# Optimization experiments

Measured on AMD Instinct MI355X. Metric: run time of the kernel, lower is better.

Reference implementation:

```python
import jax, jax.numpy as jnp
import numpy as np
import math

CHANNELS = 1024
NUM_HEADS = 16
HEAD_DIM = CHANNELS // NUM_HEADS  # 64
ROPE_DIM = int(HEAD_DIM * 0.5)    # 32
BASE_FREQ = 10000.0


def apply_rope(x):
    """x: [b, h, t, d]; rotate first ROPE_DIM features, pass the rest through."""
    t = x.shape[2]
    half = ROPE_DIM // 2
    theta = 1.0 / (BASE_FREQ ** (jnp.arange(0, ROPE_DIM, 2, dtype=jnp.float32) / ROPE_DIM))  # [half]
    ang = jnp.arange(t, dtype=jnp.float32)[:, None] * theta[None, :]  # [t, half]
    ang = jnp.concatenate([ang, ang], axis=-1)  # [t, ROPE_DIM]
    cos = jnp.cos(ang)[None, None, :, :]
    sin = jnp.sin(ang)[None, None, :, :]
    x_rope, x_pass = x[..., :ROPE_DIM], x[..., ROPE_DIM:]
    neg_half = jnp.concatenate([-x_rope[..., half:], x_rope[..., :half]], axis=-1)
    x_rope = x_rope * cos + neg_half * sin
    return jnp.concatenate([x_rope, x_pass], axis=-1)


def proximal_bias(length):
    pos = jnp.arange(length, dtype=jnp.float32)
    diff = pos[None, :] - pos[:, None]
    return -jnp.log1p(jnp.abs(diff))[None, None, :, :]  # [1,1,t,t]


def conv1x1(x, w, b):
    """x: [b, c_in, t], w: [c_out, c_in], b: [c_out] -> [b, c_out, t]"""
    return jnp.einsum('oc,bct->bot', w, x) + b[None, :, None]


def setup_inputs() -> dict:
    key = jax.random.key(0)
    ks = jax.random.split(key, 10)
    B, C, T = 8, CHANNELS, 1024
    scale = 1.0 / math.sqrt(C)
    return {
        "x": jax.random.normal(ks[0], (B, C, T), dtype=jnp.float32),
        "context": jax.random.normal(ks[1], (B, C, T), dtype=jnp.float32),
        "attention_mask": jnp.ones((B, 1, 1, T), dtype=jnp.int32),
        "Wq": jax.random.normal(ks[2], (C, C), dtype=jnp.float32) * scale,
        "bq": jnp.zeros((C,), dtype=jnp.float32),
        "Wk": jax.random.normal(ks[3], (C, C), dtype=jnp.float32) * scale,
        "bk": jnp.zeros((C,), dtype=jnp.float32),
        "Wv": jax.random.normal(ks[4], (C, C), dtype=jnp.float32) * scale,
        "bv": jnp.zeros((C,), dtype=jnp.float32),
        "Wo": jax.random.normal(ks[5], (C, C), dtype=jnp.float32) * scale,
        "bo": jnp.zeros((C,), dtype=jnp.float32),
    }


def reference(x, context, attention_mask, Wq, bq, Wk, bk, Wv, bv, Wo, bo):
    B, C, T = x.shape
    H, D = NUM_HEADS, HEAD_DIM
    q = conv1x1(x, Wq, bq)
    k = conv1x1(context, Wk, bk)
    v = conv1x1(context, Wv, bv)
    # b (h d) t -> b h t d
    def split_heads(z):
        return z.reshape(B, H, D, -1).transpose(0, 1, 3, 2)
    q, k, v = split_heads(q), split_heads(k), split_heads(v)
    q = apply_rope(q)
    k = apply_rope(k)
    scores = jnp.einsum('bhqd,bhkd->bhqk', q, k) / math.sqrt(D)
    scores = scores + proximal_bias(T)  # proximal_bias=True, self-attention
    scores = jnp.where(attention_mask == 0, jnp.float32(-10000.0), scores)
    probs = jax.nn.softmax(scores, axis=-1)  # dropout_rate=0.0 -> identity
    out = jnp.einsum('bhqk,bhkd->bhqd', probs, v)
    # b h q d -> b (h d) q
    out = out.transpose(0, 1, 3, 2).reshape(B, C, T)
    return conv1x1(out, Wo, bo)
```

## Files before the change

kernel.cpp:

```cpp
#include <hip/hip_runtime.h>
#include <hip/hip_bf16.h>
#include <math.h>

#define BB 8
#define CC 1024
#define TT 1024
#define HH 16
#define DD 64

typedef __attribute__((ext_vector_type(8))) short short8;
typedef __attribute__((ext_vector_type(4))) short short4_;
typedef __attribute__((ext_vector_type(4))) float f32x4;
typedef __attribute__((ext_vector_type(4))) int   i32x4;
typedef __attribute__((ext_vector_type(2))) unsigned long long u64x2;

#define QSCALE 0.18033688f

__device__ __forceinline__ unsigned short f2bf(float f) {
    unsigned u = __builtin_bit_cast(unsigned, f);
    u += 0x7fffu + ((u >> 16) & 1u);
    return (unsigned short)(u >> 16);
}

__device__ __forceinline__ f32x4 mfma16(short8 a, short8 b, f32x4 c) {
    return __builtin_amdgcn_mfma_f32_16x16x32_bf16(a, b, c, 0, 0, 0);
}

__device__ __forceinline__ void async16(const void* g, void* l) {
    __builtin_amdgcn_global_load_lds(
        (const __attribute__((address_space(1))) unsigned int*)g,
        (__attribute__((address_space(3))) unsigned int*)l, 16, 0, 0);
}

__device__ __forceinline__ unsigned cvtpk(float lo, float hi) {
    unsigned r;
    asm("v_cvt_pk_bf16_f32 %0, %1, %2" : "=v"(r) : "v"(lo), "v"(hi));
    return r;
}

__global__ __launch_bounds__(256) void cast_w_kernel(
    const float* __restrict__ Wq, const float* __restrict__ Wk,
    const float* __restrict__ Wv, const float* __restrict__ Wo,
    unsigned short* __restrict__ dst)
{
    const int z = blockIdx.y;
    const float* W = (z == 0) ? Wq : (z == 1) ? Wk : (z == 2) ? Wv : Wo;
    unsigned short* d = dst + (size_t)z * CC * CC;
    int idx = blockIdx.x * 256 + threadIdx.x;
    float4 f = ((const float4*)W)[idx];
    short4_ s;
    s[0] = (short)f2bf(f.x); s[1] = (short)f2bf(f.y);
    s[2] = (short)f2bf(f.z); s[3] = (short)f2bf(f.w);
    ((short4_*)d)[idx] = s;
}

__global__ __launch_bounds__(256) void tcast2_kernel(
    const float* __restrict__ x, const float* __restrict__ ctx,
    unsigned short* __restrict__ xT, unsigned short* __restrict__ cTo)
{
    __shared__ float sT[64][65];
    const int tid = threadIdx.x;
    const int z = blockIdx.z;
    const float* in = (z < BB) ? x : ctx;
    unsigned short* out = (z < BB) ? xT : cTo;
    const int b = (z < BB) ? z : z - BB;
    const int tB = blockIdx.x * 64, cT = blockIdx.y * 64;

    const float* ib = in + ((size_t)b * CC + cT) * TT + tB;
    const int r = tid >> 2;
    #pragma unroll
    for (int j = 0; j < 4; j++) {
        int t4 = (tid & 3) * 4 + j * 16;
        float4 f = *(const float4*)(ib + (size_t)r * TT + t4);
        sT[r][t4 + 0] = f.x; sT[r][t4 + 1] = f.y;
        sT[r][t4 + 2] = f.z; sT[r][t4 + 3] = f.w;
    }
    __syncthreads();
    const int t_l = tid >> 2, cch = (tid & 3) * 16;
    short8 o0, o1;
    #pragma unroll
    for (int i = 0; i < 8; i++) {
        o0[i] = (short)f2bf(sT[cch + i][t_l]);
        o1[i] = (short)f2bf(sT[cch + 8 + i][t_l]);
    }
    unsigned short* dp = out + ((size_t)b * TT + tB + t_l) * CC + cT + cch;
    *(short8*)dp = o0;
    *(short8*)(dp + 8) = o1;
}

__global__ __launch_bounds__(256) void tcast_kernel(
    const float* __restrict__ in, unsigned short* __restrict__ out)
{
    __shared__ float sT[64][65];
    const int tid = threadIdx.x;
    const int tB = blockIdx.x * 64, cT = blockIdx.y * 64, b = blockIdx.z;

    const float* ib = in + ((size_t)b * CC + cT) * TT + tB;
    const int r = tid >> 2;
    #pragma unroll
    for (int j = 0; j < 4; j++) {
        int t4 = (tid & 3) * 4 + j * 16;
        float4 f = *(const float4*)(ib + (size_t)r * TT + t4);
        sT[r][t4 + 0] = f.x; sT[r][t4 + 1] = f.y;
        sT[r][t4 + 2] = f.z; sT[r][t4 + 3] = f.w;
    }
    __syncthreads();
    const int t_l = tid >> 2, cch = (tid & 3) * 16;
    short8 o0, o1;
    #pragma unroll
    for (int i = 0; i < 8; i++) {
        o0[i] = (short)f2bf(sT[cch + i][t_l]);
        o1[i] = (short)f2bf(sT[cch + 8 + i][t_l]);
    }
    unsigned short* dp = out + ((size_t)b * TT + tB + t_l) * CC + cT + cch;
    *(short8*)dp = o0;
    *(short8*)(dp + 8) = o1;
}

__global__ __launch_bounds__(256) void qkv_gll_kernel(
    const unsigned short* __restrict__ xT, const unsigned short* __restrict__ cT,
    const unsigned short* __restrict__ Wq2, const unsigned short* __restrict__ Wk2,
    const unsigned short* __restrict__ Wv2,
    const float* __restrict__ bq, const float* __restrict__ bk,
    const float* __restrict__ bv,
    unsigned short* __restrict__ qo, unsigned short* __restrict__ ko,
    unsigned short* __restrict__ vo,
    int mode)
{
    __shared__ __align__(16) short smem[4 * 64 * 72];
    short* sA = smem;
    short* sB = smem + 4096;

    const int tid = threadIdx.x, lane = tid & 63, wave = tid >> 6;
    const int wm = wave >> 1, wn = wave & 1;
    const int l15 = lane & 15, lq = lane >> 4;

    const int tTile = blockIdx.x, oTile = blockIdx.y;
    const int zz = blockIdx.z;
    int w, b;
    if (mode == 0)      { w = zz % 3;        b = zz / 3;  }
    else if (mode == 1) { w = 0;             b = zz;      }
    else                { w = 1 + (zz & 1);  b = zz >> 1; }
    const unsigned short* inT = (w == 0) ? xT : cT;
    const int oBase = oTile * 128, tBase = tTile * 128;

    const unsigned short* WA = (w == 0) ? Wq2 : (w == 1) ? Wk2 : Wv2;
    const float* bias        = (w == 0) ? bq  : (w == 1) ? bk  : bv;

    const int srow = lane >> 2;
    const int sch  = (lane ^ (lane >> 2) ^ (lane >> 4)) & 3;
    const unsigned short* gA0 = WA + (size_t)(oBase + wave * 32 + srow) * CC + sch * 8;
    const unsigned short* gA1 = gA0 + (size_t)16 * CC;
    const unsigned short* gB0 = inT + ((size_t)b * TT + tBase + wave * 32 + srow) * CC + sch * 8;
    const unsigned short* gB1 = gB0 + (size_t)16 * CC;
    short* lA0 = sA + (wave * 2 + 0) * 512;
    short* lA1 = sA + (wave * 2 + 1) * 512;
    short* lB0 = sB + (wave * 2 + 0) * 512;
    short* lB1 = sB + (wave * 2 + 1) * 512;

    const int csw = ((lq ^ (l15 & 3) ^ (l15 >> 2)) & 3) * 8;

    f32x4 acc[4][4];
    #pragma unroll
    for (int mt = 0; mt < 4; mt++)
        #pragma unroll
        for (int nt = 0; nt < 4; nt++) acc[mt][nt] = (f32x4){0.f, 0.f, 0.f, 0.f};

    for (int c0 = 0; c0 < CC; c0 += 32) {
        async16(gA0 + c0, lA0);
        async16(gA1 + c0, lA1);
        async16(gB0 + c0, lB0);
        async16(gB1 + c0, lB1);
        __syncthreads();

        short8 af[4], bf[4];
        #pragma unroll
        for (int mt = 0; mt < 4; mt++)
            af[mt] = *(short8*)(sA + (wm * 64 + mt * 16 + l15) * 32 + csw);
        #pragma unroll
        for (int nt = 0; nt < 4; nt++)
            bf[nt] = *(short8*)(sB + (wn * 64 + nt * 16 + l15) * 32 + csw);
        #pragma unroll
        for (int mt = 0; mt < 4; mt++)
            #pragma unroll
            for (int nt = 0; nt < 4; nt++)
                acc[mt][nt] = mfma16(af[mt], bf[nt], acc[mt][nt]);
        __syncthreads();
    }

    #pragma unroll
    for (int mt = 0; mt < 4; mt++)
        #pragma unroll
        for (int r = 0; r < 4; r++) {
            float bi = bias[oBase + wm * 64 + mt * 16 + lq * 4 + r];
            #pragma unroll
            for (int nt = 0; nt < 4; nt++) {
                acc[mt][nt][r] += bi;
                if (w == 0) acc[mt][nt][r] *= QSCALE;
            }
        }

    const int h = oTile * 2 + wm;
    short* sT = smem + wave * (64 * 72);

    if (w < 2) {
        #pragma unroll
        for (int r = 0; r < 4; r++) {
            float dr = (float)(lq * 4 + r);
            float theta = exp2f(dr * -0.8304820237f);
            float sa, ca, ss, cs;
            sincosf((float)(tBase + wn * 64 + l15) * theta, &sa, &ca);
            sincosf(16.0f * theta, &ss, &cs);
            #pragma unroll
            for (int nt = 0; nt < 4; nt++) {
                float x0 = acc[0][nt][r], x1 = acc[1][nt][r];
                acc[0][nt][r] = x0 * ca - x1 * sa;
                acc[1][nt][r] = x1 * ca + x0 * sa;
                float c2 = ca * cs - sa * ss;
                sa = sa * cs + ca * ss;
                ca = c2;
            }
        }
        #pragma unroll
        for (int nt = 0; nt < 4; nt++)
            #pragma unroll
            for (int mt = 0; mt < 4; mt++) {
                short4_ v4;
                #pragma unroll
                for (int r = 0; r < 4; r++) v4[r] = (short)f2bf(acc[mt][nt][r]);
                *(short4_*)(sT + (nt * 16 + l15) * 72 + mt * 16 + lq * 4) = v4;
            }
    } else {
        #pragma unroll
        for (int mt = 0; mt < 4; mt++)
            #pragma unroll
            for (int r = 0; r < 4; r++)
                #pragma unroll
                for (int nt = 0; nt < 4; nt++)
                    sT[(mt * 16 + lq * 4 + r) * 72 + nt * 16 + l15] =
                        (short)f2bf(acc[mt][nt][r]);
    }
    __asm__ volatile("s_waitcnt lgkmcnt(0)" ::: "memory");

    unsigned short* dstBase;
    if (w == 0)
        dstBase = qo + ((size_t)(b * HH + h) * TT + tBase + wn * 64 + lane) * DD;
    else if (w == 1)
        dstBase = ko + ((size_t)(b * HH + h) * TT + tBase + wn * 64 + lane) * DD;
    else
        dstBase = vo + ((size_t)(b * HH + h) * DD + lane) * TT + tBase + wn * 64;
    #pragma unroll
    for (int j = 0; j < 8; j++)
        *(short8*)(dstBase + j * 8) = *(short8*)(sT + lane * 72 + j * 8);
}

__global__ __launch_bounds__(256) void oproj_gll_kernel(
    const unsigned short* __restrict__ att, const unsigned short* __restrict__ Wo2,
    const float* __restrict__ bo, float* __restrict__ out)
{
    __shared__ __align__(16) short smem[8192];
    short* sA = smem;
    short* sB = smem + 4096;

    const int tid = threadIdx.x, lane = tid & 63, wave = tid >> 6;
    const int wm = wave >> 1, wn = wave & 1;
    const int l15 = lane & 15, lq = lane >> 4;
    const int tTile = blockIdx.x, oTile = blockIdx.y, b = blockIdx.z;
    const int oBase = oTile * 128, tBase = tTile * 128;

    const int srow = lane >> 2;
    const int sch  = (lane ^ (lane >> 2) ^ (lane >> 4)) & 3;
    const unsigned short* gA0 = Wo2 + (size_t)(oBase + wave * 32 + srow) * CC + sch * 8;
    const unsigned short* gA1 = gA0 + (size_t)16 * CC;
    const unsigned short* attB = att + (size_t)b * HH * TT * DD;
    const int t0 = tBase + wave * 32 + srow;
    short* lA0 = sA + (wave * 2 + 0) * 512;
    short* lA1 = sA + (wave * 2 + 1) * 512;
    short* lB0 = sB + (wave * 2 + 0) * 512;
    short* lB1 = sB + (wave * 2 + 1) * 512;

    const int csw = ((lq ^ (l15 & 3) ^ (l15 >> 2)) & 3) * 8;

    f32x4 acc[4][4];
    #pragma unroll
    for (int mt = 0; mt < 4; mt++)
        #pragma unroll
        for (int nt = 0; nt < 4; nt++) acc[mt][nt] = (f32x4){0.f, 0.f, 0.f, 0.f};

    for (int c0 = 0; c0 < CC; c0 += 32) {
        int c = c0 + sch * 8;
        const unsigned short* g0 =
            attB + ((size_t)(c >> 6) * TT + t0) * DD + (c & 63);
        async16(gA0 + c0, lA0);
        async16(gA1 + c0, lA1);
        async16(g0, lB0);
        async16(g0 + 16 * DD, lB1);
        __syncthreads();

        short8 af[4], bf[4];
        #pragma unroll
        for (int mt = 0; mt < 4; mt++)
            af[mt] = *(short8*)(sA + (wm * 64 + mt * 16 + l15) * 32 + csw);
        #pragma unroll
        for (int nt = 0; nt < 4; nt++)
            bf[nt] = *(short8*)(sB + (wn * 64 + nt * 16 + l15) * 32 + csw);
        #pragma unroll
        for (int mt = 0; mt < 4; mt++)
            #pragma unroll
            for (int nt = 0; nt < 4; nt++)
                acc[mt][nt] = mfma16(af[mt], bf[nt], acc[mt][nt]);
        __syncthreads();
    }

    #pragma unroll
    for (int mt = 0; mt < 4; mt++)
        #pragma unroll
        for (int r = 0; r < 4; r++) {
            int o = oBase + wm * 64 + mt * 16 + lq * 4 + r;
            float bi = bo[o];
            float* dst = out + ((size_t)b * CC + o) * TT + tBase + wn * 64;
            #pragma unroll
            for (int nt = 0; nt < 4; nt++)
                dst[nt * 16 + l15] = acc[mt][nt][r] + bi;
        }
}

__global__ __launch_bounds__(256) void attn_mfma_kernel(
    const unsigned short* __restrict__ q, const unsigned short* __restrict__ k,
    const unsigned short* __restrict__ v, const int* __restrict__ mask,
    unsigned short* __restrict__ att)
{
    __shared__ __align__(16) short sQw[64 * 72];
    __shared__ __align__(16) short sK[64 * 72];
    __shared__ __align__(16) short sV[64 * 72];
    __shared__ int sOK[4];

    const int tid = threadIdx.x, lane = tid & 63, wq = tid >> 6;
    const int l15 = lane & 15, lq = lane >> 4;
    const int qTile = blockIdx.x, bh = blockIdx.y, b = bh >> 4;

    const int sr = tid >> 2, sc = (tid & 3) * 16;
    const int* maskB = mask + b * TT;

    {
        i32x4 m4 = *(const i32x4*)(maskB + tid * 4);
        int ok = (m4[0] != 0) & (m4[1] != 0) & (m4[2] != 0) & (m4[3] != 0);
        unsigned long long bal = __ballot(ok);
        if (lane == 0) sOK[wq] = (bal == ~0ull);
    }

    {
        const unsigned short* gq = q + ((size_t)bh * TT + qTile * 64 + sr) * DD + sc;
        *(short8*)(sQw + sr * 72 + sc)     = *(const short8*)gq;
        *(short8*)(sQw + sr * 72 + sc + 8) = *(const short8*)(gq + 8);
    }
    __syncthreads();

    const short8 bq0 = *(short8*)(sQw + (wq * 16 + l15) * 72 + lq * 8);
    const short8 bq1 = *(short8*)(sQw + (wq * 16 + l15) * 72 + 32 + lq * 8);
    const bool allOK = sOK[0] && sOK[1] && sOK[2] && sOK[3];
    __syncthreads();

    float* wtab = (float*)sQw;
    #pragma unroll
    for (int j = 0; j < 8; j++) {
        int d = tid + 256 * j;
        int ad = d - 1023; ad = ad < 0 ? -ad : ad;
        wtab[d] = __builtin_amdgcn_rcpf(1.0f + (float)ad);
    }

    short8 vones;
    #pragma unroll
    for (int e = 0; e < 8; e++) vones[e] = (short)0x3F80;

    f32x4 accO[4];
    #pragma unroll
    for (int nt = 0; nt < 4; nt++) accO[nt] = (f32x4){0.f, 0.f, 0.f, 0.f};
    f32x4 accD = (f32x4){0.f, 0.f, 0.f, 0.f};

    const int qpos = qTile * 64 + wq * 16 + l15;
    const unsigned short* kB = k + (size_t)bh * TT * DD;
    const unsigned short* vB = v + (size_t)bh * DD * TT;

    const int xo = ((tid & 3) >> 1) * 8 + (tid & 1) * 4;
    short* vwp = sV + sr * 72 + xo;

    const unsigned short* gk = kB + (size_t)sr * DD + sc;
    const unsigned short* gv = vB + (size_t)sr * TT + sc;
    short8 kr0 = *(const short8*)gk;
    short8 kr1 = *(const short8*)(gk + 8);
    short8 vr0 = *(const short8*)gv;
    short8 vr1 = *(const short8*)(gv + 8);

    for (int kt = 0; kt < 16; kt++) {
        __syncthreads();
        *(short8*)(sK + sr * 72 + sc)     = kr0;
        *(short8*)(sK + sr * 72 + sc + 8) = kr1;
        {
            u64x2 vv0 = __builtin_bit_cast(u64x2, vr0);
            u64x2 vv1 = __builtin_bit_cast(u64x2, vr1);
            *(unsigned long long*)(vwp)      = vv0[0];
            *(unsigned long long*)(vwp + 16) = vv0[1];
            *(unsigned long long*)(vwp + 32) = vv1[0];
            *(unsigned long long*)(vwp + 48) = vv1[1];
        }
        __syncthreads();

        if (kt < 15) {
            gk += 64 * DD;
            gv += 64;
            kr0 = *(const short8*)gk;
            kr1 = *(const short8*)(gk + 8);
            vr0 = *(const short8*)gv;
            vr1 = *(const short8*)(gv + 8);
        }

        f32x4 s4[4];
        #pragma unroll
        for (int nt = 0; nt < 4; nt++) {
            short8 ka0 = *(short8*)(sK + (nt * 16 + l15) * 72 + lq * 8);
            short8 ka1 = *(short8*)(sK + (nt * 16 + l15) * 72 + 32 + lq * 8);
            f32x4 z = (f32x4){0.f, 0.f, 0.f, 0.f};
            z = mfma16(ka0, bq0, z);
            z = mfma16(ka1, bq1, z);
            s4[nt] = z;
        }

        const float* wrow = wtab + (kt * 64 + lq * 4 + 1023 - qpos);
        unsigned pk8[4][2];
        if (allOK) {
            #pragma unroll
            for (int nt = 0; nt < 4; nt++) {
                #pragma unroll
                for (int h2 = 0; h2 < 2; h2++) {
                    float p0 = __builtin_amdgcn_exp2f(s4[nt][2 * h2])
                               * wrow[nt * 16 + 2 * h2];
                    float p1 = __builtin_amdgcn_exp2f(s4[nt][2 * h2 + 1])
                               * wrow[nt * 16 + 2 * h2 + 1];
                    pk8[nt][h2] = cvtpk(p0, p1);
                }
            }
        } else {
            #pragma unroll
            for (int nt = 0; nt < 4; nt++) {
                i32x4 mk = *(const i32x4*)(maskB + kt * 64 + nt * 16 + lq * 4);
                #pragma unroll
                for (int h2 = 0; h2 < 2; h2++) {
                    float p0 = __builtin_amdgcn_exp2f(s4[nt][2 * h2])
                               * wrow[nt * 16 + 2 * h2];
                    float p1 = __builtin_amdgcn_exp2f(s4[nt][2 * h2 + 1])
                               * wrow[nt * 16 + 2 * h2 + 1];
                    p0 = mk[2 * h2]     ? p0 : 0.f;
                    p1 = mk[2 * h2 + 1] ? p1 : 0.f;
                    pk8[nt][h2] = cvtpk(p0, p1);
                }
            }
        }

        i32x4 c0 = {(int)pk8[0][0], (int)pk8[0][1], (int)pk8[1][0], (int)pk8[1][1]};
        i32x4 c1 = {(int)pk8[2][0], (int)pk8[2][1], (int)pk8[3][0], (int)pk8[3][1]};
        short8 ap0 = __builtin_bit_cast(short8, c0);
        short8 ap1 = __builtin_bit_cast(short8, c1);

        accD = mfma16(ap0, vones, accD);
        accD = mfma16(ap1, vones, accD);

        #pragma unroll
        for (int nt = 0; nt < 4; nt++) {
            const short* vrow = sV + (nt * 16 + l15) * 72 + lq * 16;
            short8 b0 = *(short8*)(vrow);
            short8 b1 = *(short8*)(vrow + 8);
            accO[nt] = mfma16(ap0, b0, accO[nt]);
            accO[nt] = mfma16(ap1, b1, accO[nt]);
        }
    }

    unsigned short* aB = att + ((size_t)bh * TT + qTile * 64 + wq * 16 + lq * 4) * DD;
    #pragma unroll
    for (int r = 0; r < 4; r++) {
        float inv = 1.0f / accD[r];
        #pragma unroll
        for (int nt = 0; nt < 4; nt++)
            aB[(size_t)r * DD + nt * 16 + l15] = f2bf(accO[nt][r] * inv);
    }
}

__global__ __launch_bounds__(256) void qkv_mfma_kernel(
    const float* __restrict__ x, const float* __restrict__ ctx,
    const float* __restrict__ Wq, const float* __restrict__ bq,
    const float* __restrict__ Wk, const float* __restrict__ bk,
    const float* __restrict__ Wv, const float* __restrict__ bv,
    unsigned short* __restrict__ qo, unsigned short* __restrict__ ko,
    unsigned short* __restrict__ vo)
{
    __shared__ __align__(16) short smem[4 * 64 * 72];
    short* sA = smem;
    short* sB = smem + 128 * 40;

    const int tid  = threadIdx.x;
    const int lane = tid & 63;
    const int wave = tid >> 6;
    const int wm = wave >> 1, wn = wave & 1;
    const int l15 = lane & 15, lq = lane >> 4;

    const int tTile = blockIdx.x, oTile = blockIdx.y;
    const int b = blockIdx.z / 3, w = blockIdx.z % 3;
    const int oBase = oTile * 128, tBase = tTile * 128;

    const float* In   = (w == 0) ? x  : ctx;
    const float* W    = (w == 0) ? Wq : (w == 1) ? Wk : Wv;
    const float* bias = (w == 0) ? bq : (w == 1) ? bk : bv;
    const float* InB  = In + (size_t)b * CC * TT;

    const int ao = tid >> 1, ak = (tid & 1) * 16;
    const int bt = tid & 127, bk_ = (tid >> 7) * 16;
    const float* gA = W + (size_t)(oBase + ao) * CC + ak;
    const float* gB = InB + (size_t)bk_ * TT + tBase + bt;

    f32x4 acc[4][4];
    #pragma unroll
    for (int mt = 0; mt < 4; mt++)
        #pragma unroll
        for (int nt = 0; nt < 4; nt++) acc[mt][nt] = (f32x4){0.f, 0.f, 0.f, 0.f};

    for (int c0 = 0; c0 < CC; c0 += 32) {
        float fa[16], fb[16];
        #pragma unroll
        for (int i = 0; i < 4; i++) {
            float4 t4 = *(const float4*)(gA + c0 + 4 * i);
            fa[4*i+0] = t4.x; fa[4*i+1] = t4.y; fa[4*i+2] = t4.z; fa[4*i+3] = t4.w;
        }
        #pragma unroll
        for (int j = 0; j < 16; j++)
            fb[j] = gB[(size_t)(c0 + j) * TT];

        __syncthreads();
        short8 pa0, pa1, pb0, pb1;
        #pragma unroll
        for (int e = 0; e < 8; e++) {
            pa0[e] = (short)f2bf(fa[e]);   pa1[e] = (short)f2bf(fa[8 + e]);
            pb0[e] = (short)f2bf(fb[e]);   pb1[e] = (short)f2bf(fb[8 + e]);
        }
        *(short8*)(sA + ao * 40 + ak)     = pa0;
        *(short8*)(sA + ao * 40 + ak + 8) = pa1;
        *(short8*)(sB + bt * 40 + bk_)     = pb0;
        *(short8*)(sB + bt * 40 + bk_ + 8) = pb1;
        __syncthreads();

        short8 af[4], bf[4];
        #pragma unroll
        for (int mt = 0; mt < 4; mt++)
            af[mt] = *(short8*)(sA + (wm * 64 + mt * 16 + l15) * 40 + lq * 8);
        #pragma unroll
        for (int nt = 0; nt < 4; nt++)
            bf[nt] = *(short8*)(sB + (wn * 64 + nt * 16 + l15) * 40 + lq * 8);
        #pragma unroll
        for (int mt = 0; mt < 4; mt++)
            #pragma unroll
            for (int nt = 0; nt < 4; nt++)
                acc[mt][nt] = mfma16(af[mt], bf[nt], acc[mt][nt]);
    }

    #pragma unroll
    for (int mt = 0; mt < 4; mt++)
        #pragma unroll
        for (int r = 0; r < 4; r++) {
            float bi = bias[oBase + wm * 64 + mt * 16 + lq * 4 + r];
            #pragma unroll
            for (int nt = 0; nt < 4; nt++) {
                acc[mt][nt][r] += bi;
                if (w == 0) acc[mt][nt][r] *= QSCALE;
            }
        }

    const int h = oTile * 2 + wm;
    __syncthreads();
    short* sT = smem + wave * (64 * 72);

    if (w < 2) {
        #pragma unroll
        for (int r = 0; r < 4; r++) {
            float theta = powf(10000.0f, -(float)(lq * 4 + r) * (1.0f / 16.0f));
            #pragma unroll
            for (int nt = 0; nt < 4; nt++) {
                float tpos = (float)(tBase + wn * 64 + nt * 16 + l15);
                float sa, ca;
                sincosf(tpos * theta, &sa, &ca);
                float x0 = acc[0][nt][r], x1 = acc[1][nt][r];
                acc[0][nt][r] = x0 * ca - x1 * sa;
                acc[1][nt][r] = x1 * ca + x0 * sa;
            }
        }
        #pragma unroll
        for (int nt = 0; nt < 4; nt++)
            #pragma unroll
            for (int mt = 0; mt < 4; mt++) {
                short4_ v4;
                #pragma unroll
                for (int r = 0; r < 4; r++) v4[r] = (short)f2bf(acc[mt][nt][r]);
                *(short4_*)(sT + (nt * 16 + l15) * 72 + mt * 16 + lq * 4) = v4;
            }
    } else {
        #pragma unroll
        for (int mt = 0; mt < 4; mt++)
            #pragma unroll
            for (int r = 0; r < 4; r++)
                #pragma unroll
                for (int nt = 0; nt < 4; nt++)
                    sT[(mt * 16 + lq * 4 + r) * 72 + nt * 16 + l15] =
                        (short)f2bf(acc[mt][nt][r]);
    }
    __asm__ volatile("s_waitcnt lgkmcnt(0)" ::: "memory");

    unsigned short* dstBase;
    if (w == 0)
        dstBase = qo + ((size_t)(b * HH + h) * TT + tBase + wn * 64 + lane) * DD;
    else if (w == 1)
        dstBase = ko + ((size_t)(b * HH + h) * TT + tBase + wn * 64 + lane) * DD;
    else
        dstBase = vo + ((size_t)(b * HH + h) * DD + lane) * TT + tBase + wn * 64;
    #pragma unroll
    for (int j = 0; j < 8; j++)
        *(short8*)(dstBase + j * 8) = *(short8*)(sT + lane * 72 + j * 8);
}

__global__ __launch_bounds__(256) void oproj_mfma_kernel(
    const unsigned short* __restrict__ att, const float* __restrict__ Wo,
    const float* __restrict__ bo, float* __restrict__ out)
{
    __shared__ __align__(16) short smem[2 * 128 * 40];
    short* sA = smem;
    short* sB = smem + 128 * 40;

    const int tid = threadIdx.x, lane = tid & 63, wave = tid >> 6;
    const int wm = wave >> 1, wn = wave & 1;
    const int l15 = lane & 15, lq = lane >> 4;
    const int tTile = blockIdx.x, oTile = blockIdx.y, b = blockIdx.z;
    const int oBase = oTile * 128, tBase = tTile * 128;

    const int ao = tid >> 1, ak = (tid & 1) * 16;
    const int bt = tid & 127, bk_ = (tid >> 7) * 16;
    const float* gA = Wo + (size_t)(oBase + ao) * CC + ak;

    f32x4 acc[4][4];
    #pragma unroll
    for (int mt = 0; mt < 4; mt++)
        #pragma unroll
        for (int nt = 0; nt < 4; nt++) acc[mt][nt] = (f32x4){0.f, 0.f, 0.f, 0.f};

    for (int c0 = 0; c0 < CC; c0 += 32) {
        float fa[16];
        #pragma unroll
        for (int i = 0; i < 4; i++) {
            float4 t4 = *(const float4*)(gA + c0 + 4 * i);
            fa[4*i+0] = t4.x; fa[4*i+1] = t4.y; fa[4*i+2] = t4.z; fa[4*i+3] = t4.w;
        }
        int c = c0 + bk_;
        const unsigned short* gB =
            att + (((size_t)b * HH + (c >> 6)) * TT + tBase + bt) * DD + (c & 63);
        short8 pb0 = *(const short8*)gB;
        short8 pb1 = *(const short8*)(gB + 8);

        __syncthreads();
        short8 pa0, pa1;
        #pragma unroll
        for (int e = 0; e < 8; e++) {
            pa0[e] = (short)f2bf(fa[e]); pa1[e] = (short)f2bf(fa[8 + e]);
        }
        *(short8*)(sA + ao * 40 + ak)      = pa0;
        *(short8*)(sA + ao * 40 + ak + 8)  = pa1;
        *(short8*)(sB + bt * 40 + bk_)     = pb0;
        *(short8*)(sB + bt * 40 + bk_ + 8) = pb1;
        __syncthreads();

        short8 af[4], bf[4];
        #pragma unroll
        for (int mt = 0; mt < 4; mt++)
            af[mt] = *(short8*)(sA + (wm * 64 + mt * 16 + l15) * 40 + lq * 8);
        #pragma unroll
        for (int nt = 0; nt < 4; nt++)
            bf[nt] = *(short8*)(sB + (wn * 64 + nt * 16 + l15) * 40 + lq * 8);
        #pragma unroll
        for (int mt = 0; mt < 4; mt++)
            #pragma unroll
            for (int nt = 0; nt < 4; nt++)
                acc[mt][nt] = mfma16(af[mt], bf[nt], acc[mt][nt]);
    }

    #pragma unroll
    for (int mt = 0; mt < 4; mt++)
        #pragma unroll
        for (int r = 0; r < 4; r++) {
            int o = oBase + wm * 64 + mt * 16 + lq * 4 + r;
            float bi = bo[o];
            float* dst = out + ((size_t)b * CC + o) * TT + tBase + wn * 64;
            #pragma unroll
            for (int nt = 0; nt < 4; nt++)
                dst[nt * 16 + l15] = acc[mt][nt][r] + bi;
        }
}

extern "C" void kernel_launch(void* const* d_in, const int* in_sizes, int n_in,
                              void* d_out, int out_size, void* d_ws, size_t ws_size,
                              hipStream_t stream)
{
    const float* x   = (const float*)d_in[0];
    const float* ctx = (const float*)d_in[1];
    const int* mask  = (const int*)d_in[2];
    const float* Wq  = (const float*)d_in[3];
    const float* bq  = (const float*)d_in[4];
    const float* Wk  = (const float*)d_in[5];
    const float* bk  = (const float*)d_in[6];
    const float* Wv  = (const float*)d_in[7];
    const float* bv  = (const float*)d_in[8];
    const float* Wo  = (const float*)d_in[9];
    const float* bo  = (const float*)d_in[10];
    float* out = (float*)d_out;

    const size_t nq = (size_t)BB * HH * TT * DD;
    const size_t nw = (size_t)CC * CC;

    if (ws_size >= (5 * nq + 4 * nw) * sizeof(unsigned short)) {
        unsigned short* q   = (unsigned short*)d_ws;
        unsigned short* k   = q + nq;
        unsigned short* v   = k + nq;
        unsigned short* xT  = v + nq;
        unsigned short* cT  = xT + nq;
        unsigned short* Wb  = cT + nq;
        unsigned short* Wqb = Wb;
        unsigned short* Wkb = Wb + nw;
        unsigned short* Wvb = Wb + 2 * nw;
        unsigned short* Wob = Wb + 3 * nw;

        cast_w_kernel<<<dim3(1024, 4), 256, 0, stream>>>(Wq, Wk, Wv, Wo, Wb);
        tcast2_kernel<<<dim3(16, 16, BB * 2), 256, 0, stream>>>(x, ctx, xT, cT);
        qkv_gll_kernel<<<dim3(8, 8, BB * 3), 256, 0, stream>>>(
            xT, cT, Wqb, Wkb, Wvb, bq, bk, bv, q, k, v, 0);
        attn_mfma_kernel<<<dim3(TT / 64, BB * HH), 256, 0, stream>>>(
            q, k, v, mask, xT);
        oproj_gll_kernel<<<dim3(8, 8, BB), 256, 0, stream>>>(xT, Wob, bo, out);
    } else if (ws_size >= (4 * nq + 4 * nw) * sizeof(unsigned short)) {
        unsigned short* q   = (unsigned short*)d_ws;
        unsigned short* k   = q + nq;
        unsigned short* v   = k + nq;
        unsigned short* buf = v + nq;
        unsigned short* Wb  = buf + nq;
        unsigned short* Wqb = Wb;
        unsigned short* Wkb = Wb + nw;
        unsigned short* Wvb = Wb + 2 * nw;
        unsigned short* Wob = Wb + 3 * nw;

        cast_w_kernel<<<dim3(1024, 4), 256, 0, stream>>>(Wq, Wk, Wv, Wo, Wb);
        tcast_kernel<<<dim3(16, 16, BB), 256, 0, stream>>>(x, buf);
        qkv_gll_kernel<<<dim3(8, 8, BB), 256, 0, stream>>>(
            buf, buf, Wqb, Wkb, Wvb, bq, bk, bv, q, k, v, 1);
        tcast_kernel<<<dim3(16, 16, BB), 256, 0, stream>>>(ctx, buf);
        qkv_gll_kernel<<<dim3(8, 8, BB * 2), 256, 0, stream>>>(
            buf, buf, Wqb, Wkb, Wvb, bq, bk, bv, q, k, v, 2);
        attn_mfma_kernel<<<dim3(TT / 64, BB * HH), 256, 0, stream>>>(
            q, k, v, mask, buf);
        oproj_gll_kernel<<<dim3(8, 8, BB), 256, 0, stream>>>(buf, Wob, bo, out);
    } else {
        unsigned short* q   = (unsigned short*)d_ws;
        unsigned short* k   = q + nq;
        unsigned short* v   = k + nq;
        unsigned short* att = v + nq;
        qkv_mfma_kernel<<<dim3(8, 8, BB * 3), 256, 0, stream>>>(
            x, ctx, Wq, bq, Wk, bk, Wv, bv, q, k, v);
        attn_mfma_kernel<<<dim3(TT / 64, BB * HH), 256, 0, stream>>>(
            q, k, v, mask, att);
        oproj_mfma_kernel<<<dim3(8, 8, BB), 256, 0, stream>>>(att, Wo, bo, out);
    }
}
```

Baseline: 304.1 us.

## Double-buffer LDS tiles in QKV and output projection GEMMs

Both projection GEMM kernels now use two LDS buffers per operand: the next K-slice is prefetched with async global-to-LDS loads while the current slice is consumed by MFMA, and buffers are swapped after a single barrier per iteration. This is meant to overlap global memory latency with compute instead of stalling on a barrier right after each load. It doubles LDS use in the output projection kernel, which may reduce occupancy, and correctness depends on the async loads completing before the next barrier.

After: 307.9 us. No clear change (+1.2%).

```diff
diff --git a/kernel.cpp b/kernel.cpp
--- a/kernel.cpp
+++ b/kernel.cpp
@@ -128,8 +128,6 @@
     int mode)
 {
     __shared__ __align__(16) short smem[4 * 64 * 72];
-    short* sA = smem;
-    short* sB = smem + 4096;
 
     const int tid = threadIdx.x, lane = tid & 63, wave = tid >> 6;
     const int wm = wave >> 1, wn = wave & 1;
@@ -153,10 +151,13 @@
     const unsigned short* gA1 = gA0 + (size_t)16 * CC;
     const unsigned short* gB0 = inT + ((size_t)b * TT + tBase + wave * 32 + srow) * CC + sch * 8;
     const unsigned short* gB1 = gB0 + (size_t)16 * CC;
-    short* lA0 = sA + (wave * 2 + 0) * 512;
-    short* lA1 = sA + (wave * 2 + 1) * 512;
-    short* lB0 = sB + (wave * 2 + 0) * 512;
-    short* lB1 = sB + (wave * 2 + 1) * 512;
+
+    short* curA = smem;
+    short* curB = smem + 4096;
+    short* nxtA = smem + 8192;
+    short* nxtB = smem + 12288;
+    const int oA0 = (wave * 2 + 0) * 512;
+    const int oA1 = (wave * 2 + 1) * 512;
 
     const int csw = ((lq ^ (l15 & 3) ^ (l15 >> 2)) & 3) * 8;
 
@@ -166,26 +167,36 @@
         #pragma unroll
         for (int nt = 0; nt < 4; nt++) acc[mt][nt] = (f32x4){0.f, 0.f, 0.f, 0.f};
 
+    async16(gA0, curA + oA0);
+    async16(gA1, curA + oA1);
+    async16(gB0, curB + oA0);
+    async16(gB1, curB + oA1);
+    __syncthreads();
+
     for (int c0 = 0; c0 < CC; c0 += 32) {
-        async16(gA0 + c0, lA0);
-        async16(gA1 + c0, lA1);
-        async16(gB0 + c0, lB0);
-        async16(gB1 + c0, lB1);
-        __syncthreads();
+        if (c0 + 32 < CC) {
+            async16(gA0 + c0 + 32, nxtA + oA0);
+            async16(gA1 + c0 + 32, nxtA + oA1);
+            async16(gB0 + c0 + 32, nxtB + oA0);
+            async16(gB1 + c0 + 32, nxtB + oA1);
+        }
 
         short8 af[4], bf[4];
         #pragma unroll
         for (int mt = 0; mt < 4; mt++)
-            af[mt] = *(short8*)(sA + (wm * 64 + mt * 16 + l15) * 32 + csw);
+            af[mt] = *(short8*)(curA + (wm * 64 + mt * 16 + l15) * 32 + csw);
         #pragma unroll
         for (int nt = 0; nt < 4; nt++)
-            bf[nt] = *(short8*)(sB + (wn * 64 + nt * 16 + l15) * 32 + csw);
+            bf[nt] = *(short8*)(curB + (wn * 64 + nt * 16 + l15) * 32 + csw);
         #pragma unroll
         for (int mt = 0; mt < 4; mt++)
             #pragma unroll
             for (int nt = 0; nt < 4; nt++)
                 acc[mt][nt] = mfma16(af[mt], bf[nt], acc[mt][nt]);
+
         __syncthreads();
+        short* t0 = curA; curA = nxtA; nxtA = t0;
+        short* t1 = curB; curB = nxtB; nxtB = t1;
     }
 
     #pragma unroll
@@ -258,9 +269,7 @@
     const unsigned short* __restrict__ att, const unsigned short* __restrict__ Wo2,
     const float* __restrict__ bo, float* __restrict__ out)
 {
-    __shared__ __align__(16) short smem[8192];
-    short* sA = smem;
-    short* sB = smem + 4096;
+    __shared__ __align__(16) short smem[16384];
 
     const int tid = threadIdx.x, lane = tid & 63, wave = tid >> 6;
     const int wm = wave >> 1, wn = wave & 1;
@@ -274,10 +283,13 @@
     const unsigned short* gA1 = gA0 + (size_t)16 * CC;
     const unsigned short* attB = att + (size_t)b * HH * TT * DD;
     const int t0 = tBase + wave * 32 + srow;
-    short* lA0 = sA + (wave * 2 + 0) * 512;
-    short* lA1 = sA + (wave * 2 + 1) * 512;
-    short* lB0 = sB + (wave * 2 + 0) * 512;
-    short* lB1 = sB + (wave * 2 + 1) * 512;
+
+    short* curA = smem;
+    short* curB = smem + 4096;
+    short* nxtA = smem + 8192;
+    short* nxtB = smem + 12288;
+    const int oA0 = (wave * 2 + 0) * 512;
+    const int oA1 = (wave * 2 + 1) * 512;
 
     const int csw = ((lq ^ (l15 & 3) ^ (l15 >> 2)) & 3) * 8;
 
@@ -287,29 +299,46 @@
         #pragma unroll
         for (int nt = 0; nt < 4; nt++) acc[mt][nt] = (f32x4){0.f, 0.f, 0.f, 0.f};
 
-    for (int c0 = 0; c0 < CC; c0 += 32) {
-        int c = c0 + sch * 8;
+    const int csch = sch * 8;
+
+    {
+        int c = csch;
         const unsigned short* g0 =
             attB + ((size_t)(c >> 6) * TT + t0) * DD + (c & 63);
-        async16(gA0 + c0, lA0);
-        async16(gA1 + c0, lA1);
-        async16(g0, lB0);
-        async16(g0 + 16 * DD, lB1);
-        __syncthreads();
+        async16(gA0, curA + oA0);
+        async16(gA1, curA + oA1);
+        async16(g0, curB + oA0);
+        async16(g0 + 16 * DD, curB + oA1);
+    }
+    __syncthreads();
+
+    for (int c0 = 0; c0 < CC; c0 += 32) {
+        if (c0 + 32 < CC) {
+            int c = c0 + 32 + csch;
+            const unsigned short* g0 =
+                attB + ((size_t)(c >> 6) * TT + t0) * DD + (c & 63);
+            async16(gA0 + c0 + 32, nxtA + oA0);
+            async16(gA1 + c0 + 32, nxtA + oA1);
+            async16(g0, nxtB + oA0);
+            async16(g0 + 16 * DD, nxtB + oA1);
+        }
 
         short8 af[4], bf[4];
         #pragma unroll
         for (int mt = 0; mt < 4; mt++)
-            af[mt] = *(short8*)(sA + (wm * 64 + mt * 16 + l15) * 32 + csw);
+            af[mt] = *(short8*)(curA + (wm * 64 + mt * 16 + l15) * 32 + csw);
         #pragma unroll
         for (int nt = 0; nt < 4; nt++)
-            bf[nt] = *(short8*)(sB + (wn * 64 + nt * 16 + l15) * 32 + csw);
+            bf[nt] = *(short8*)(curB + (wn * 64 + nt * 16 + l15) * 32 + csw);
         #pragma unroll
         for (int mt = 0; mt < 4; mt++)
             #pragma unroll
             for (int nt = 0; nt < 4; nt++)
                 acc[mt][nt] = mfma16(af[mt], bf[nt], acc[mt][nt]);
+
         __syncthreads();
+        short* s0 = curA; curA = nxtA; nxtA = s0;
+        short* s1 = curB; curB = nxtB; nxtB = s1;
     }
 
     #pragma unroll
```

## Double-buffer LDS in QKV and output-projection GEMMs and reorder grid dimensions

Applied to the files above, without the earlier changes.

Both the QKV and output-projection GEMM loops now use two LDS buffers, so the global-to-LDS async load for the next K-slice is issued while MFMAs run on the current one. This replaces the two __syncthreads per 32-wide step with one barrier per step, using explicit waitcnt and sched_barrier. Separately, the grid axes are permuted in all three kernels so that batch/head indices vary fastest, which changes which blocks run together and how they share data in L2. LDS use doubles in the projection kernels, which may lower occupancy.

New measurement: 303.3 us. Within noise of the previous version (-0.3%).

```diff
diff --git a/kernel.cpp b/kernel.cpp
--- a/kernel.cpp
+++ b/kernel.cpp
@@ -128,15 +128,12 @@
     int mode)
 {
     __shared__ __align__(16) short smem[4 * 64 * 72];
-    short* sA = smem;
-    short* sB = smem + 4096;
 
     const int tid = threadIdx.x, lane = tid & 63, wave = tid >> 6;
     const int wm = wave >> 1, wn = wave & 1;
     const int l15 = lane & 15, lq = lane >> 4;
 
-    const int tTile = blockIdx.x, oTile = blockIdx.y;
-    const int zz = blockIdx.z;
+    const int zz = blockIdx.x, tTile = blockIdx.y, oTile = blockIdx.z;
     int w, b;
     if (mode == 0)      { w = zz % 3;        b = zz / 3;  }
     else if (mode == 1) { w = 0;             b = zz;      }
@@ -153,10 +150,11 @@
     const unsigned short* gA1 = gA0 + (size_t)16 * CC;
     const unsigned short* gB0 = inT + ((size_t)b * TT + tBase + wave * 32 + srow) * CC + sch * 8;
     const unsigned short* gB1 = gB0 + (size_t)16 * CC;
-    short* lA0 = sA + (wave * 2 + 0) * 512;
-    short* lA1 = sA + (wave * 2 + 1) * 512;
-    short* lB0 = sB + (wave * 2 + 0) * 512;
-    short* lB1 = sB + (wave * 2 + 1) * 512;
+
+    short* A0b = smem;            short* B0b = smem + 4096;
+    short* A1b = smem + 8192;     short* B1b = smem + 12288;
+    const int oA0 = (wave * 2 + 0) * 512;
+    const int oA1 = (wave * 2 + 1) * 512;
 
     const int csw = ((lq ^ (l15 & 3) ^ (l15 >> 2)) & 3) * 8;
 
@@ -166,27 +164,47 @@
         #pragma unroll
         for (int nt = 0; nt < 4; nt++) acc[mt][nt] = (f32x4){0.f, 0.f, 0.f, 0.f};
 
-    for (int c0 = 0; c0 < CC; c0 += 32) {
-        async16(gA0 + c0, lA0);
-        async16(gA1 + c0, lA1);
-        async16(gB0 + c0, lB0);
-        async16(gB1 + c0, lB1);
-        __syncthreads();
-
+    auto stage = [&](int c0, short* dA, short* dB) {
+        async16(gA0 + c0, dA + oA0);
+        async16(gA1 + c0, dA + oA1);
+        async16(gB0 + c0, dB + oA0);
+        async16(gB1 + c0, dB + oA1);
+    };
+    auto compute = [&](const short* bA, const short* bB) {
         short8 af[4], bf[4];
         #pragma unroll
         for (int mt = 0; mt < 4; mt++)
-            af[mt] = *(short8*)(sA + (wm * 64 + mt * 16 + l15) * 32 + csw);
+            af[mt] = *(const short8*)(bA + (wm * 64 + mt * 16 + l15) * 32 + csw);
         #pragma unroll
         for (int nt = 0; nt < 4; nt++)
-            bf[nt] = *(short8*)(sB + (wn * 64 + nt * 16 + l15) * 32 + csw);
+            bf[nt] = *(const short8*)(bB + (wn * 64 + nt * 16 + l15) * 32 + csw);
         #pragma unroll
         for (int mt = 0; mt < 4; mt++)
             #pragma unroll
             for (int nt = 0; nt < 4; nt++)
                 acc[mt][nt] = mfma16(af[mt], bf[nt], acc[mt][nt]);
-        __syncthreads();
-    }
+    };
+
+    stage(0, A0b, B0b);
+
+    #pragma unroll 1
+    for (int tt = 0; tt < 16; tt++) {
+        const int c = tt * 64;
+        asm volatile("s_waitcnt vmcnt(0)" ::: "memory");
+        __builtin_amdgcn_s_barrier();
+        __builtin_amdgcn_sched_barrier(0);
+        stage(c + 32, A1b, B1b);
+        compute(A0b, B0b);
+        asm volatile("s_waitcnt lgkmcnt(0)" ::: "memory");
+
+        asm volatile("s_waitcnt vmcnt(0)" ::: "memory");
+        __builtin_amdgcn_s_barrier();
+        __builtin_amdgcn_sched_barrier(0);
+        if (tt < 15) stage(c + 64, A0b, B0b);
+        compute(A1b, B1b);
+        asm volatile("s_waitcnt lgkmcnt(0)" ::: "memory");
+    }
+    __syncthreads();
 
     #pragma unroll
     for (int mt = 0; mt < 4; mt++)
@@ -258,14 +276,12 @@
     const unsigned short* __restrict__ att, const unsigned short* __restrict__ Wo2,
     const float* __restrict__ bo, float* __restrict__ out)
 {
-    __shared__ __align__(16) short smem[8192];
-    short* sA = smem;
-    short* sB = smem + 4096;
+    __shared__ __align__(16) short smem[16384];
 
     const int tid = threadIdx.x, lane = tid & 63, wave = tid >> 6;
     const int wm = wave >> 1, wn = wave & 1;
     const int l15 = lane & 15, lq = lane >> 4;
-    const int tTile = blockIdx.x, oTile = blockIdx.y, b = blockIdx.z;
+    const int b = blockIdx.x, tTile = blockIdx.y, oTile = blockIdx.z;
     const int oBase = oTile * 128, tBase = tTile * 128;
 
     const int srow = lane >> 2;
@@ -274,10 +290,12 @@
     const unsigned short* gA1 = gA0 + (size_t)16 * CC;
     const unsigned short* attB = att + (size_t)b * HH * TT * DD;
     const int t0 = tBase + wave * 32 + srow;
-    short* lA0 = sA + (wave * 2 + 0) * 512;
-    short* lA1 = sA + (wave * 2 + 1) * 512;
-    short* lB0 = sB + (wave * 2 + 0) * 512;
-    short* lB1 = sB + (wave * 2 + 1) * 512;
+    const int csch = sch * 8;
+
+    short* A0b = smem;            short* B0b = smem + 4096;
+    short* A1b = smem + 8192;     short* B1b = smem + 12288;
+    const int oA0 = (wave * 2 + 0) * 512;
+    const int oA1 = (wave * 2 + 1) * 512;
 
     const int csw = ((lq ^ (l15 & 3) ^ (l15 >> 2)) & 3) * 8;
 
@@ -287,29 +305,48 @@
         #pragma unroll
         for (int nt = 0; nt < 4; nt++) acc[mt][nt] = (f32x4){0.f, 0.f, 0.f, 0.f};
 
-    for (int c0 = 0; c0 < CC; c0 += 32) {
-        int c = c0 + sch * 8;
+    auto stage = [&](int c0, short* dA, short* dB) {
+        int c = c0 + csch;
         const unsigned short* g0 =
             attB + ((size_t)(c >> 6) * TT + t0) * DD + (c & 63);
-        async16(gA0 + c0, lA0);
-        async16(gA1 + c0, lA1);
-        async16(g0, lB0);
-        async16(g0 + 16 * DD, lB1);
-        __syncthreads();
-
+        async16(gA0 + c0, dA + oA0);
+        async16(gA1 + c0, dA + oA1);
+        async16(g0, dB + oA0);
+        async16(g0 + 16 * DD, dB + oA1);
+    };
+    auto compute = [&](const short* bA, const short* bB) {
         short8 af[4], bf[4];
         #pragma unroll
         for (int mt = 0; mt < 4; mt++)
-            af[mt] = *(short8*)(sA + (wm * 64 + mt * 16 + l15) * 32 + csw);
+            af[mt] = *(const short8*)(bA + (wm * 64 + mt * 16 + l15) * 32 + csw);
         #pragma unroll
         for (int nt = 0; nt < 4; nt++)
-            bf[nt] = *(short8*)(sB + (wn * 64 + nt * 16 + l15) * 32 + csw);
+            bf[nt] = *(const short8*)(bB + (wn * 64 + nt * 16 + l15) * 32 + csw);
         #pragma unroll
         for (int mt = 0; mt < 4; mt++)
             #pragma unroll
             for (int nt = 0; nt < 4; nt++)
                 acc[mt][nt] = mfma16(af[mt], bf[nt], acc[mt][nt]);
-        __syncthreads();
+    };
+
+    stage(0, A0b, B0b);
+
+    #pragma unroll 1
+    for (int tt = 0; tt < 16; tt++) {
+        const int c = tt * 64;
+        asm volatile("s_waitcnt vmcnt(0)" ::: "memory");
+        __builtin_amdgcn_s_barrier();
+        __builtin_amdgcn_sched_barrier(0);
+        stage(c + 32, A1b, B1b);
+        compute(A0b, B0b);
+        asm volatile("s_waitcnt lgkmcnt(0)" ::: "memory");
+
+        asm volatile("s_waitcnt vmcnt(0)" ::: "memory");
+        __builtin_amdgcn_s_barrier();
+        __builtin_amdgcn_sched_barrier(0);
+        if (tt < 15) stage(c + 64, A0b, B0b);
+        compute(A1b, B1b);
+        asm volatile("s_waitcnt lgkmcnt(0)" ::: "memory");
     }
 
     #pragma unroll
@@ -337,7 +374,7 @@
 
     const int tid = threadIdx.x, lane = tid & 63, wq = tid >> 6;
     const int l15 = lane & 15, lq = lane >> 4;
-    const int qTile = blockIdx.x, bh = blockIdx.y, b = bh >> 4;
+    const int bh = blockIdx.x, qTile = blockIdx.y, b = bh >> 4;
 
     const int sr = tid >> 2, sc = (tid & 3) * 16;
     const int* maskB = mask + b * TT;
@@ -734,11 +771,11 @@
 
         cast_w_kernel<<<dim3(1024, 4), 256, 0, stream>>>(Wq, Wk, Wv, Wo, Wb);
         tcast2_kernel<<<dim3(16, 16, BB * 2), 256, 0, stream>>>(x, ctx, xT, cT);
-        qkv_gll_kernel<<<dim3(8, 8, BB * 3), 256, 0, stream>>>(
+        qkv_gll_kernel<<<dim3(BB * 3, 8, 8), 256, 0, stream>>>(
             xT, cT, Wqb, Wkb, Wvb, bq, bk, bv, q, k, v, 0);
-        attn_mfma_kernel<<<dim3(TT / 64, BB * HH), 256, 0, stream>>>(
+        attn_mfma_kernel<<<dim3(BB * HH, TT / 64), 256, 0, stream>>>(
             q, k, v, mask, xT);
-        oproj_gll_kernel<<<dim3(8, 8, BB), 256, 0, stream>>>(xT, Wob, bo, out);
+        oproj_gll_kernel<<<dim3(BB, 8, 8), 256, 0, stream>>>(xT, Wob, bo, out);
     } else if (ws_size >= (4 * nq + 4 * nw) * sizeof(unsigned short)) {
         unsigned short* q   = (unsigned short*)d_ws;
         unsigned short* k   = q + nq;
@@ -752,14 +789,14 @@
 
         cast_w_kernel<<<dim3(1024, 4), 256, 0, stream>>>(Wq, Wk, Wv, Wo, Wb);
         tcast_kernel<<<dim3(16, 16, BB), 256, 0, stream>>>(x, buf);
-        qkv_gll_kernel<<<dim3(8, 8, BB), 256, 0, stream>>>(
+        qkv_gll_kernel<<<dim3(BB, 8, 8), 256, 0, stream>>>(
             buf, buf, Wqb, Wkb, Wvb, bq, bk, bv, q, k, v, 1);
         tcast_kernel<<<dim3(16, 16, BB), 256, 0, stream>>>(ctx, buf);
-        qkv_gll_kernel<<<dim3(8, 8, BB * 2), 256, 0, stream>>>(
+        qkv_gll_kernel<<<dim3(BB * 2, 8, 8), 256, 0, stream>>>(
             buf, buf, Wqb, Wkb, Wvb, bq, bk, bv, q, k, v, 2);
-        attn_mfma_kernel<<<dim3(TT / 64, BB * HH), 256, 0, stream>>>(
+        attn_mfma_kernel<<<dim3(BB * HH, TT / 64), 256, 0, stream>>>(
             q, k, v, mask, buf);
-        oproj_gll_kernel<<<dim3(8, 8, BB), 256, 0, stream>>>(buf, Wob, bo, out);
+        oproj_gll_kernel<<<dim3(BB, 8, 8), 256, 0, stream>>>(buf, Wob, bo, out);
     } else {
         unsigned short* q   = (unsigned short*)d_ws;
         unsigned short* k   = q + nq;
@@ -767,7 +804,7 @@
         unsigned short* att = v + nq;
         qkv_mfma_kernel<<<dim3(8, 8, BB * 3), 256, 0, stream>>>(
             x, ctx, Wq, bq, Wk, bk, Wv, bv, q, k, v);
-        attn_mfma_kernel<<<dim3(TT / 64, BB * HH), 256, 0, stream>>>(
+        attn_mfma_kernel<<<dim3(BB * HH, TT / 64), 256, 0, stream>>>(
             q, k, v, mask, att);
         oproj_mfma_kernel<<<dim3(8, 8, BB), 256, 0, stream>>>(att, Wo, bo, out);
     }
```
